# Kernel optimization log

Measured on AMD Instinct MI355X. Metric: run time of the kernel, lower is better.

Reference implementation:

```python
import jax, jax.numpy as jnp
import numpy as np

SCALING = 32.0 / 16.0  # alpha / rank


def setup_inputs() -> dict:
    key = jax.random.key(0)
    k1, k2, k3, k4, k5 = jax.random.split(key, 5)
    B_, S, D_in, D_out, R = 4, 2048, 4096, 4096, 16
    x = jax.random.normal(k1, (B_, S, D_in), dtype=jnp.float32)
    W = jax.random.normal(k2, (D_out, D_in), dtype=jnp.float32) * (1.0 / np.sqrt(D_in))
    b = jax.random.normal(k3, (D_out,), dtype=jnp.float32) * 0.02
    lora_A = jax.random.normal(k4, (R, D_in), dtype=jnp.float32) * (1.0 / np.sqrt(D_in))
    lora_B = jax.random.normal(k5, (D_out, R), dtype=jnp.float32) * 0.02
    return {"x": x, "W": W, "b": b, "lora_A": lora_A, "lora_B": lora_B}


def reference(x, W, b, lora_A, lora_B):
    # Base linear: y = x @ W^T + b
    base = jnp.einsum('bsd,od->bso', x, W) + b
    # LoRA path: ((x @ A^T) @ B^T) * scaling  (dropout=0 -> identity)
    xa = jnp.einsum('bsd,rd->bsr', x, lora_A)      # [B,S,r]
    lora = jnp.einsum('bsr,or->bso', xa, lora_B)    # [B,S,D_out]
    return base + lora * SCALING
```

## Files before the change

### kernel.cpp

```cpp
#include <hip/hip_runtime.h>
#include <hip/hip_bf16.h>
#include <stdint.h>

typedef __bf16 bf16x8 __attribute__((ext_vector_type(8)));
typedef float  f32x4  __attribute__((ext_vector_type(4)));
typedef unsigned short u16x8 __attribute__((ext_vector_type(8)));


__device__ __forceinline__ unsigned short f32_to_bf16_rne(float f) {
  union { float f; unsigned int u; } v; v.f = f;
  unsigned int u = v.u;
  unsigned int r = u + 0x7fffu + ((u >> 16) & 1u);
  return (unsigned short)(r >> 16);
}

__device__ __forceinline__ void async16(const unsigned short* g, unsigned short* l) {
  __builtin_amdgcn_global_load_lds(
      (const __attribute__((address_space(1))) unsigned int*)g,
      (__attribute__((address_space(3))) unsigned int*)l,
      16, 0, 0);
}

__global__ __launch_bounds__(256) void prep_fused(const float* __restrict__ W,
                                                  const float* __restrict__ lA,
                                                  const float* __restrict__ lB,
                                                  const float* __restrict__ x,
                                                  unsigned short* __restrict__ Wp,
                                                  unsigned short* __restrict__ xb) {
  const int b   = blockIdx.x;
  const int tid = threadIdx.x;
  if (b < 2048) {
    const int ro = (b & 511) * 8;
    const int k  = (b >> 9) * 1024 + tid * 4;
    float4 a[16];
    #pragma unroll
    for (int r = 0; r < 16; ++r)
      a[r] = *(const float4*)(lA + (size_t)r * 4096 + k);
    #pragma unroll
    for (int i = 0; i < 8; ++i) {
      const int o = ro + i;
      float4 acc = *(const float4*)(W + (size_t)o * 4096 + k);
      #pragma unroll
      for (int r = 0; r < 16; ++r) {
        const float s = lB[o * 16 + r] * 2.0f;
        acc.x += s * a[r].x; acc.y += s * a[r].y;
        acc.z += s * a[r].z; acc.w += s * a[r].w;
      }
      ushort4 ov;
      ov.x = f32_to_bf16_rne(acc.x);
      ov.y = f32_to_bf16_rne(acc.y);
      ov.z = f32_to_bf16_rne(acc.z);
      ov.w = f32_to_bf16_rne(acc.w);
      *(ushort4*)(Wp + (size_t)o * 4096 + k) = ov;
    }
  } else {
    const int cb = b - 2048;
    #pragma unroll
    for (int it = 0; it < 4; ++it) {
      const size_t g8 = (size_t)cb * 1024 + it * 256 + tid;
      const float4* p = (const float4*)x + g8 * 2;
      const float4 f0 = p[0], f1 = p[1];
      u16x8 o;
      o[0] = f32_to_bf16_rne(f0.x); o[1] = f32_to_bf16_rne(f0.y);
      o[2] = f32_to_bf16_rne(f0.z); o[3] = f32_to_bf16_rne(f0.w);
      o[4] = f32_to_bf16_rne(f1.x); o[5] = f32_to_bf16_rne(f1.y);
      o[6] = f32_to_bf16_rne(f1.z); o[7] = f32_to_bf16_rne(f1.w);
      *((u16x8*)xb + g8) = o;
    }
  }
}

#define BM 128
#define BN 128
#define BK 32
#define GEMM_M 8192
#define GEMM_N 4096
#define GEMM_K 4096

template <bool A_F32>
__global__ __launch_bounds__(256) void gemm_bias(
    const void* __restrict__ Aptr,
    const unsigned short* __restrict__ B,
    const float* __restrict__ bias,
    float* __restrict__ C) {
  __shared__ __align__(16) unsigned short sA[BM * BK];
  __shared__ __align__(16) unsigned short sB[BM * BK];

  const int tid  = threadIdx.x;
  const int wave = tid >> 6;
  const int lane = tid & 63;

  const int srow = tid >> 2;
  const int scol = (tid & 3) << 3;

  const size_t a_row0 = (size_t)blockIdx.y * BM;
  const size_t b_row0 = (size_t)blockIdx.x * BN;

  const unsigned short* bg0 = B + (b_row0 +      srow) * GEMM_K + scol;
  const unsigned short* bg1 = B + (b_row0 + 64 + srow) * GEMM_K + scol;

  unsigned short* sA0 = sA +        wave * 512;
  unsigned short* sA1 = sA + 2048 + wave * 512;
  unsigned short* sB0 = sB +        wave * 512;
  unsigned short* sB1 = sB + 2048 + wave * 512;

  const unsigned short* ag0 = nullptr; const unsigned short* ag1 = nullptr;
  const float* af0 = nullptr; const float* af1 = nullptr;
  if constexpr (A_F32) {
    af0 = (const float*)Aptr + (a_row0 +      srow) * GEMM_K + scol;
    af1 = (const float*)Aptr + (a_row0 + 64 + srow) * GEMM_K + scol;
  } else {
    ag0 = (const unsigned short*)Aptr + (a_row0 +      srow) * GEMM_K + scol;
    ag1 = (const unsigned short*)Aptr + (a_row0 + 64 + srow) * GEMM_K + scol;
  }
  unsigned short* sAw0 = sA +        tid * 8;
  unsigned short* sAw1 = sA + 2048 + tid * 8;

  const int wm   = (wave >> 1) * 64;
  const int wn   = (wave & 1) * 64;
  const int lrow = lane & 15;
  const int lk   = (lane >> 4) * 8;

  const unsigned short* sa_rd = sA + (wm + lrow) * BK + lk;
  const unsigned short* sb_rd = sB + (wn + lrow) * BK + lk;

  f32x4 acc[4][4];
  #pragma unroll
  for (int i = 0; i < 4; ++i)
    #pragma unroll
    for (int j = 0; j < 4; ++j)
      acc[i][j] = (f32x4){0.f, 0.f, 0.f, 0.f};

  for (int k0 = 0; k0 < GEMM_K; k0 += BK) {
    __syncthreads();
    async16(bg0 + k0, sB0);
    async16(bg1 + k0, sB1);
    if constexpr (A_F32) {
      const float* p0 = af0 + k0;
      const float* p1 = af1 + k0;
      const float4 x0 = *(const float4*)(p0);
      const float4 x1 = *(const float4*)(p0 + 4);
      const float4 y0 = *(const float4*)(p1);
      const float4 y1 = *(const float4*)(p1 + 4);
      u16x8 w0, w1;
      w0[0] = f32_to_bf16_rne(x0.x); w0[1] = f32_to_bf16_rne(x0.y);
      w0[2] = f32_to_bf16_rne(x0.z); w0[3] = f32_to_bf16_rne(x0.w);
      w0[4] = f32_to_bf16_rne(x1.x); w0[5] = f32_to_bf16_rne(x1.y);
      w0[6] = f32_to_bf16_rne(x1.z); w0[7] = f32_to_bf16_rne(x1.w);
      w1[0] = f32_to_bf16_rne(y0.x); w1[1] = f32_to_bf16_rne(y0.y);
      w1[2] = f32_to_bf16_rne(y0.z); w1[3] = f32_to_bf16_rne(y0.w);
      w1[4] = f32_to_bf16_rne(y1.x); w1[5] = f32_to_bf16_rne(y1.y);
      w1[6] = f32_to_bf16_rne(y1.z); w1[7] = f32_to_bf16_rne(y1.w);
      *(u16x8*)sAw0 = w0;
      *(u16x8*)sAw1 = w1;
    } else {
      async16(ag0 + k0, sA0);
      async16(ag1 + k0, sA1);
    }
    __syncthreads();

    bf16x8 af[4], bf[4];
    #pragma unroll
    for (int i = 0; i < 4; ++i) {
      af[i] = *(const bf16x8*)(sa_rd + i * 16 * BK);
      bf[i] = *(const bf16x8*)(sb_rd + i * 16 * BK);
    }
    #pragma unroll
    for (int i = 0; i < 4; ++i)
      #pragma unroll
      for (int j = 0; j < 4; ++j)
        acc[i][j] = __builtin_amdgcn_mfma_f32_16x16x32_bf16(af[i], bf[j], acc[i][j], 0, 0, 0);
  }

  const int row0 = (int)a_row0 + wm + (lane >> 4) * 4;
  const int col0 = (int)b_row0 + wn + lrow;
  float bv[4];
  #pragma unroll
  for (int j = 0; j < 4; ++j) bv[j] = bias[col0 + j * 16];
  #pragma unroll
  for (int i = 0; i < 4; ++i)
    #pragma unroll
    for (int j = 0; j < 4; ++j) {
      const int col = col0 + j * 16;
      #pragma unroll
      for (int r = 0; r < 4; ++r) {
        const int row = row0 + i * 16 + r;
        C[(size_t)row * GEMM_N + col] = acc[i][j][r] + bv[j];
      }
    }
}


extern "C" void kernel_launch(void* const* d_in, const int* in_sizes, int n_in,
                              void* d_out, int out_size, void* d_ws, size_t ws_size,
                              hipStream_t stream) {
  const float* x  = (const float*)d_in[0];
  const float* W  = (const float*)d_in[1];
  const float* b  = (const float*)d_in[2];
  const float* lA = (const float*)d_in[3];
  const float* lB = (const float*)d_in[4];
  float* out = (float*)d_out;
  (void)in_sizes; (void)n_in; (void)out_size;

  const size_t WP_BYTES = (size_t)4096 * 4096 * 2;
  const size_t XB_BYTES = (size_t)8192 * 4096 * 2;
  unsigned short* Wp = (unsigned short*)d_ws;

  if (ws_size >= WP_BYTES + XB_BYTES) {
    unsigned short* xb = Wp + (size_t)4096 * 4096;
    prep_fused<<<6144, 256, 0, stream>>>(W, lA, lB, x, Wp, xb);
    gemm_bias<false><<<dim3(GEMM_N / BN, GEMM_M / BM), 256, 0, stream>>>(
        (const void*)xb, Wp, b, out);
  } else {
    prep_fused<<<2048, 256, 0, stream>>>(W, lA, lB, x, Wp, (unsigned short*)nullptr);
    gemm_bias<true><<<dim3(GEMM_N / BN, GEMM_M / BM), 256, 0, stream>>>(
        (const void*)x, Wp, b, out);
  }
}
```

Measured before the change: 574.2 us.

## Replace bf16 GEMM with 256x256 tile, 8-wave double-buffered pipelined kernel

Adds a new GEMM kernel that uses 256x256 output tiles with BK=64, 8 waves per block, and double-buffered LDS. Global-to-LDS async loads for future K-tiles are interleaved between MFMA phases. It also adds an XOR swizzle on the LDS layout to avoid bank conflicts, block-id swizzling for L2 locality, and s_setprio around MFMA bursts. The aim is to raise data reuse and hide memory latency behind compute, replacing the single-buffered 128x128 kernel that synchronizes twice per BK=32 step. The cost is heavier register pressure from 32 accumulators per lane, 128KB of LDS, and fragile hand-placed waitcnt and barriers.

```diff
diff --git a/kernel.cpp b/kernel.cpp
--- a/kernel.cpp
+++ b/kernel.cpp
@@ -191,6 +191,163 @@
 }
 
 
+__device__ __forceinline__ bf16x8 lds_ld(const unsigned short* p) {
+  return *(const bf16x8*)p;
+}
+
+template <int MLO>
+__device__ __forceinline__ void mfma16(f32x4 acc[8][4],
+                                       bf16x8 a0, bf16x8 a1, bf16x8 a2, bf16x8 a3,
+                                       const bf16x8 (&bf)[4][2]) {
+#pragma unroll
+  for (int n = 0; n < 4; ++n) {
+    acc[MLO][n]     = __builtin_amdgcn_mfma_f32_16x16x32_bf16(a0, bf[n][0], acc[MLO][n], 0, 0, 0);
+    acc[MLO][n]     = __builtin_amdgcn_mfma_f32_16x16x32_bf16(a1, bf[n][1], acc[MLO][n], 0, 0, 0);
+    acc[MLO + 1][n] = __builtin_amdgcn_mfma_f32_16x16x32_bf16(a2, bf[n][0], acc[MLO + 1][n], 0, 0, 0);
+    acc[MLO + 1][n] = __builtin_amdgcn_mfma_f32_16x16x32_bf16(a3, bf[n][1], acc[MLO + 1][n], 0, 0, 0);
+  }
+}
+
+#define BARRIER() asm volatile("s_barrier" ::: "memory")
+#define LGKM0()   asm volatile("s_waitcnt lgkmcnt(0)" ::: "memory")
+#define VM6()     asm volatile("s_waitcnt vmcnt(6)" ::: "memory")
+#define VM0()     asm volatile("s_waitcnt vmcnt(0)" ::: "memory")
+
+__global__ __launch_bounds__(512, 2) void gemm8p(
+    const unsigned short* __restrict__ A,
+    const unsigned short* __restrict__ B,
+    const float* __restrict__ bias,
+    float* __restrict__ C) {
+  __shared__ __align__(16) unsigned short sA[2 * 256 * 64];
+  __shared__ __align__(16) unsigned short sB[2 * 256 * 64];
+
+  const int tid  = threadIdx.x;
+  const int w    = tid >> 6;
+  const int lane = tid & 63;
+  const int wm2  = w >> 2;
+  const int wn4  = w & 3;
+  const int l15  = lane & 15;
+  const int l16  = lane >> 4;
+  const int l7   = lane & 7;
+
+  const int id  = (int)blockIdx.x;
+  const int swz = (id & 7) * 64 + (id >> 3);
+  const int by  = swz >> 4;
+  const int bx  = swz & 15;
+
+  const size_t a_row0 = (size_t)by * 256;
+  const size_t b_row0 = (size_t)bx * 256;
+
+  const int srow = w * 8 + (lane >> 3);
+  const int scol = (l7 ^ (lane >> 3)) * 8;
+  const unsigned short* Ag = A + (a_row0 + srow) * (size_t)4096 + scol;
+  const unsigned short* Bg = B + (b_row0 + srow) * (size_t)4096 + scol;
+  unsigned short* sAw = sA + w * 512;
+  unsigned short* sBw = sB + w * 512;
+
+  const int offk0 = l15 * 64 + ((l16    ) ^ l7) * 8;
+  const int offk1 = l15 * 64 + ((4 + l16) ^ l7) * 8;
+
+  f32x4 acc[8][4];
+  #pragma unroll
+  for (int i = 0; i < 8; ++i)
+    #pragma unroll
+    for (int j = 0; j < 4; ++j) acc[i][j] = (f32x4){0.f, 0.f, 0.f, 0.f};
+
+#define STAGE_A(t, cr, buf) async16(Ag + (size_t)(cr) * 4096 + (t) * 64, sAw + (buf) * 16384 + (cr) * 64)
+#define STAGE_B(t, cr, buf) async16(Bg + (size_t)(cr) * 4096 + (t) * 64, sBw + (buf) * 16384 + (cr) * 64)
+
+  STAGE_B(0, 0, 0); STAGE_B(0, 64, 0); STAGE_B(0, 128, 0); STAGE_B(0, 192, 0);
+  STAGE_A(0, 0, 0); STAGE_A(0, 64, 0); STAGE_A(0, 128, 0); STAGE_A(0, 192, 0);
+  STAGE_B(1, 0, 1); STAGE_B(1, 64, 1); STAGE_B(1, 128, 1); STAGE_B(1, 192, 1);
+  STAGE_A(1, 0, 1); STAGE_A(1, 128, 1);
+  VM6();
+  BARRIER();
+
+  for (int T = 0; T < 64; ++T) {
+    const int cb = T & 1, nb = cb ^ 1;
+    const unsigned short* sAh = sA + cb * 16384 + wm2 * 8192;
+    const unsigned short* sBh = sB + cb * 16384 + wn4 * 4096;
+    const bool pre1 = (T + 1 < 64);
+    const bool pre2 = (T + 2 < 64);
+    bf16x8 bf[4][2];
+    bf16x8 a0, a1, a2, a3;
+
+    a0 = lds_ld(sAh + 0 * 1024 + offk0);
+    a1 = lds_ld(sAh + 0 * 1024 + offk1);
+    a2 = lds_ld(sAh + 1 * 1024 + offk0);
+    a3 = lds_ld(sAh + 1 * 1024 + offk1);
+    #pragma unroll
+    for (int n = 0; n < 4; ++n) {
+      bf[n][0] = lds_ld(sBh + n * 1024 + offk0);
+      bf[n][1] = lds_ld(sBh + n * 1024 + offk1);
+    }
+    if (pre1) { STAGE_A(T + 1, 64, nb); STAGE_A(T + 1, 192, nb); }
+    BARRIER();
+    LGKM0();
+    __builtin_amdgcn_s_setprio(1);
+    mfma16<0>(acc, a0, a1, a2, a3, bf);
+    __builtin_amdgcn_s_setprio(0);
+    BARRIER();
+
+    a0 = lds_ld(sAh + 2 * 1024 + offk0);
+    a1 = lds_ld(sAh + 2 * 1024 + offk1);
+    a2 = lds_ld(sAh + 3 * 1024 + offk0);
+    a3 = lds_ld(sAh + 3 * 1024 + offk1);
+    if (pre2) { STAGE_B(T + 2, 0, cb); STAGE_B(T + 2, 64, cb); }
+    BARRIER();
+    LGKM0();
+    __builtin_amdgcn_s_setprio(1);
+    mfma16<2>(acc, a0, a1, a2, a3, bf);
+    __builtin_amdgcn_s_setprio(0);
+    BARRIER();
+
+    a0 = lds_ld(sAh + 4 * 1024 + offk0);
+    a1 = lds_ld(sAh + 4 * 1024 + offk1);
+    a2 = lds_ld(sAh + 5 * 1024 + offk0);
+    a3 = lds_ld(sAh + 5 * 1024 + offk1);
+    if (pre2) { STAGE_B(T + 2, 128, cb); STAGE_B(T + 2, 192, cb); }
+    BARRIER();
+    LGKM0();
+    __builtin_amdgcn_s_setprio(1);
+    mfma16<4>(acc, a0, a1, a2, a3, bf);
+    __builtin_amdgcn_s_setprio(0);
+    BARRIER();
+
+    a0 = lds_ld(sAh + 6 * 1024 + offk0);
+    a1 = lds_ld(sAh + 6 * 1024 + offk1);
+    a2 = lds_ld(sAh + 7 * 1024 + offk0);
+    a3 = lds_ld(sAh + 7 * 1024 + offk1);
+    if (pre2) { STAGE_A(T + 2, 0, cb); STAGE_A(T + 2, 128, cb); }
+    BARRIER();
+    LGKM0();
+    __builtin_amdgcn_s_setprio(1);
+    mfma16<6>(acc, a0, a1, a2, a3, bf);
+    __builtin_amdgcn_s_setprio(0);
+    if (T < 62) { VM6(); } else { VM0(); }
+    BARRIER();
+  }
+
+  const int erow = (int)a_row0 + wm2 * 128 + l16 * 4;
+  const int ecol = (int)b_row0 + wn4 * 64 + l15;
+  float bv[4];
+  #pragma unroll
+  for (int n = 0; n < 4; ++n) bv[n] = bias[ecol + n * 16];
+  #pragma unroll
+  for (int m = 0; m < 8; ++m)
+    #pragma unroll
+    for (int n = 0; n < 4; ++n) {
+      const int col = ecol + n * 16;
+      #pragma unroll
+      for (int r = 0; r < 4; ++r)
+        C[(size_t)(erow + m * 16 + r) * 4096 + col] = acc[m][n][r] + bv[n];
+    }
+}
+
+#undef STAGE_A
+#undef STAGE_B
+
+
 extern "C" void kernel_launch(void* const* d_in, const int* in_sizes, int n_in,
                               void* d_out, int out_size, void* d_ws, size_t ws_size,
                               hipStream_t stream) {
@@ -209,8 +366,7 @@
   if (ws_size >= WP_BYTES + XB_BYTES) {
     unsigned short* xb = Wp + (size_t)4096 * 4096;
     prep_fused<<<6144, 256, 0, stream>>>(W, lA, lB, x, Wp, xb);
-    gemm_bias<false><<<dim3(GEMM_N / BN, GEMM_M / BM), 256, 0, stream>>>(
-        (const void*)xb, Wp, b, out);
+    gemm8p<<<512, 512, 0, stream>>>(xb, Wp, b, out);
   } else {
     prep_fused<<<2048, 256, 0, stream>>>(W, lA, lB, x, Wp, (unsigned short*)nullptr);
     gemm_bias<true><<<dim3(GEMM_N / BN, GEMM_M / BM), 256, 0, stream>>>(
```

New measurement: 552.2 us. 3.8% less time.
